# Performance work log

Measured on AMD Instinct MI355X. Metric: run time of the kernel, lower is better.

Reference implementation:

```python
import jax, jax.numpy as jnp
import numpy as np

N_NODES = 800_000
N_FRAGS = 100_000
N_ROOTS = 2_000
NODE_FEATS = 86
HIDDEN = 128
MAX_BROKEN = 6
OUT_DIM = MAX_BROKEN * 2 + 1  # 13
MLP_IN = HIDDEN * 3 + OUT_DIM  # 397


def _lin_init(key, fan_in, fan_out):
    k1, k2 = jax.random.split(key)
    bound = 1.0 / np.sqrt(fan_in)
    W = jax.random.uniform(k1, (fan_in, fan_out), jnp.float32, -bound, bound)
    b = jax.random.uniform(k2, (fan_out,), jnp.float32, -bound, bound)
    return W, b


def setup_inputs() -> dict:
    key = jax.random.key(0)
    ks = jax.random.split(key, 16)
    node_h = jax.random.normal(ks[0], (N_NODES, NODE_FEATS), jnp.float32)
    segment_ids = jnp.sort(jax.random.randint(ks[1], (N_NODES,), 0, N_FRAGS))
    root_repr = jax.random.normal(ks[2], (N_ROOTS, NODE_FEATS), jnp.float32)
    ind_maps = jax.random.randint(ks[3], (N_FRAGS,), 0, N_ROOTS)
    broken = jax.random.randint(ks[4], (N_FRAGS,), 0, OUT_DIM)
    W_root, b_root = _lin_init(ks[5], NODE_FEATS, HIDDEN)
    W_in, b_in = _lin_init(ks[6], NODE_FEATS, HIDDEN)
    W_g1, b_g1 = _lin_init(ks[7], HIDDEN, HIDDEN)
    W_g2, b_g2 = _lin_init(ks[8], HIDDEN, HIDDEN)
    W_m1, b_m1 = _lin_init(ks[9], MLP_IN, HIDDEN)
    W_m2, b_m2 = _lin_init(ks[10], HIDDEN, HIDDEN)
    W_out, b_out = _lin_init(ks[11], HIDDEN, OUT_DIM)
    W_attn, b_attn = _lin_init(ks[12], HIDDEN, OUT_DIM)
    return dict(node_h=node_h, segment_ids=segment_ids, root_repr=root_repr,
                ind_maps=ind_maps, broken=broken,
                W_root=W_root, b_root=b_root, W_in=W_in, b_in=b_in,
                W_g1=W_g1, b_g1=b_g1, W_g2=W_g2, b_g2=b_g2,
                W_m1=W_m1, b_m1=b_m1, W_m2=W_m2, b_m2=b_m2,
                W_out=W_out, b_out=b_out, W_attn=W_attn, b_attn=b_attn)


def _segment_mean(x, seg_ids, num_segments):
    sums = jax.ops.segment_sum(x, seg_ids, num_segments=num_segments)
    counts = jax.ops.segment_sum(jnp.ones((x.shape[0],), x.dtype), seg_ids,
                                 num_segments=num_segments)
    return sums / jnp.maximum(counts, 1.0)[:, None]


def reference(node_h, segment_ids, root_repr, ind_maps, broken,
              W_root, b_root, W_in, b_in, W_g1, b_g1, W_g2, b_g2,
              W_m1, b_m1, W_m2, b_m2, W_out, b_out, W_attn, b_attn):
    # root encoder: Linear + ReLU (dropout=0)
    root_emb = jax.nn.relu(root_repr @ W_root + b_root)        # [R, H]
    ext_root = root_emb[ind_maps]                              # [F, H] gather
    # node input + 2 GNN (nodewise Linear+ReLU fallback) layers
    frag_h = node_h @ W_in + b_in                              # [N, H]
    frag_h = jax.nn.relu(frag_h @ W_g1 + b_g1)
    frag_h = jax.nn.relu(frag_h @ W_g2 + b_g2)
    # ragged mean-pool per fragment graph (dgl.mean_nodes)
    avg_frags = _segment_mean(frag_h, segment_ids, N_FRAGS)    # [F, H]
    # one-hot of clamped broken-bond counts
    broken_oh = jax.nn.one_hot(jnp.clip(broken, 0, MAX_BROKEN * 2), OUT_DIM,
                               dtype=frag_h.dtype)             # [F, 13]
    cat = jnp.concatenate([ext_root, ext_root - avg_frags, avg_frags,
                           broken_oh], axis=-1)                # [F, 397]
    hidden = jax.nn.relu(jax.nn.relu(cat @ W_m1 + b_m1) @ W_m2 + b_m2)
    output = jax.nn.sigmoid(hidden @ W_out + b_out)            # [F, 13]
    attn_weights = hidden @ W_attn + b_attn                    # [F, 13]
    return output, attn_weights
```

## Files before the change

### kernel.cpp

```cpp
#include <hip/hip_runtime.h>
#include <math.h>

typedef __attribute__((ext_vector_type(8))) short short8;
typedef __attribute__((ext_vector_type(4))) float float4v;

__device__ __forceinline__ unsigned short f2bf(float f) {
    union { float f; unsigned u; } v; v.f = f;
    return (unsigned short)((v.u + 0x7fffu + ((v.u >> 16) & 1u)) >> 16);
}

template<int KP>
__device__ __forceinline__ void mfma_gemm(const unsigned short* acts, int astr,
                                          const unsigned short* __restrict__ WT,
                                          const float* __restrict__ bias,
                                          unsigned short* wbuf, int tid,
                                          float4v acc[8])
{
    const int lane = tid & 63, w = tid >> 6, col0 = lane & 15, q = lane >> 4;
#pragma unroll
    for (int t = 0; t < 8; ++t) {
        float b = bias[t * 16 + col0];
        acc[t] = (float4v){b, b, b, b};
    }
    const unsigned short* arow = acts + (w * 16 + col0) * astr + q * 8;
    for (int kc = 0; kc < KP; kc += 64) {
        const int CS = (KP - kc) < 64 ? (KP - kc) : 64;
        __syncthreads();
        const int tpr = CS >> 3;
        for (int it = tid; it < 128 * tpr; it += 256) {
            int c = it / tpr, kk = (it - c * tpr) << 3;
            *(float4*)(wbuf + c * 72 + kk) =
                *(const float4*)(WT + (size_t)c * KP + kc + kk);
        }
        __syncthreads();
        for (int ks = 0; ks < CS; ks += 32) {
            short8 a = *(const short8*)(arow + kc + ks);
#pragma unroll
            for (int t = 0; t < 8; ++t) {
                short8 b = *(const short8*)(wbuf + (t * 16 + col0) * 72 + ks + q * 8);
                acc[t] = __builtin_amdgcn_mfma_f32_16x16x32_bf16(a, b, acc[t], 0, 0, 0);
            }
        }
    }
}

__device__ __forceinline__ void store_bf16(const float4v acc[8], unsigned short* out,
                                           int ostr, int tid, bool relu)
{
    const int lane = tid & 63, w = tid >> 6, col0 = lane & 15, q = lane >> 4;
#pragma unroll
    for (int t = 0; t < 8; ++t)
#pragma unroll
        for (int r = 0; r < 4; ++r) {
            float v = acc[t][r];
            if (relu) v = fmaxf(v, 0.0f);
            out[(w * 16 + q * 4 + r) * ostr + t * 16 + col0] = f2bf(v);
        }
}

__global__ void prep_kernel(const float* __restrict__ W_in, const float* __restrict__ W_g1,
                            const float* __restrict__ W_g2, const float* __restrict__ W_m1,
                            const float* __restrict__ W_m2, const float* __restrict__ W_out,
                            const float* __restrict__ W_attn, unsigned short* __restrict__ wt)
{
    int i = blockIdx.x * 256 + threadIdx.x;
    unsigned short* WT_in = wt;
    unsigned short* WT_g1 = WT_in + 12288;
    unsigned short* WT_g2 = WT_g1 + 16384;
    unsigned short* WT_m1 = WT_g2 + 16384;
    unsigned short* WT_m2 = WT_m1 + 53248;
    unsigned short* WT_h  = WT_m2 + 16384;
    if (i < 12288) { int n = i / 96, k = i - n * 96;
        WT_in[i] = (k < 86) ? f2bf(W_in[k * 128 + n]) : 0; return; }
    i -= 12288;
    if (i < 16384) { int n = i >> 7, k = i & 127;
        WT_g1[i] = f2bf(W_g1[k * 128 + n]); return; }
    i -= 16384;
    if (i < 16384) { int n = i >> 7, k = i & 127;
        WT_g2[i] = f2bf(W_g2[k * 128 + n]); return; }
    i -= 16384;
    if (i < 53248) { int n = i / 416, k = i - n * 416;
        WT_m1[i] = (k < 397) ? f2bf(W_m1[k * 128 + n]) : 0; return; }
    i -= 53248;
    if (i < 16384) { int n = i >> 7, k = i & 127;
        WT_m2[i] = f2bf(W_m2[k * 128 + n]); return; }
    i -= 16384;
    if (i < 4096) { int n = i >> 7, k = i & 127;
        WT_h[i] = (n < 13) ? f2bf(W_out[k * 13 + n])
                           : (n < 26 ? f2bf(W_attn[k * 13 + (n - 13)]) : 0); }
}

__global__ void root_kernel(const float* __restrict__ root_repr,
                            const float* __restrict__ W_root,
                            const float* __restrict__ b_root,
                            float* __restrict__ root_emb)
{
    __shared__ float x[86];
    const int r = blockIdx.x, tid = threadIdx.x;
    if (tid < 86) x[tid] = root_repr[(size_t)r * 86 + tid];
    __syncthreads();
    float acc = b_root[tid];
    for (int k = 0; k < 86; ++k)
        acc = fmaf(x[k], W_root[k * 128 + tid], acc);
    root_emb[(size_t)r * 128 + tid] = fmaxf(acc, 0.0f);
}

__global__ __launch_bounds__(256, 3)
void node_kernel(const float* __restrict__ node_h, const int* __restrict__ seg_ids,
                 const unsigned short* __restrict__ WT_in, const float* __restrict__ b_in,
                 const unsigned short* __restrict__ WT_g1, const float* __restrict__ b_g1,
                 const unsigned short* __restrict__ WT_g2, const float* __restrict__ b_g2,
                 float* __restrict__ frag_sum, float* __restrict__ frag_cnt)
{
    __shared__ __align__(16) unsigned char smem[53248];
    __shared__ int segs[64];
    unsigned short* wbuf = (unsigned short*)smem;
    unsigned short* P1   = (unsigned short*)(smem + 18432);
    unsigned short* P0   = (unsigned short*)(smem + 35840);
    float* finalF = (float*)smem;

    const int tid = threadIdx.x;
    const long n0 = (long)blockIdx.x * 64;

    if (tid < 64) {
        int s = seg_ids[n0 + tid];
        segs[tid] = s;
        atomicAdd(&frag_cnt[s], 1.0f);
    }
    for (int idx = tid; idx < 64 * 86; idx += 256) {
        int n = idx / 86, k = idx - n * 86;
        P0[n * 104 + k] = f2bf(node_h[(n0 + n) * 86 + k]);
    }
    for (int idx = tid; idx < 64 * 10; idx += 256) {
        int n = idx / 10, k = idx - n * 10;
        P0[n * 104 + 86 + k] = 0;
    }
    float4v acc[8];
    mfma_gemm<96>(P0, 104, WT_in, b_in, wbuf, tid, acc);
    store_bf16(acc, P1, 136, tid, false);
    mfma_gemm<128>(P1, 136, WT_g1, b_g1, wbuf, tid, acc);
    store_bf16(acc, P0, 136, tid, true);
    mfma_gemm<128>(P0, 136, WT_g2, b_g2, wbuf, tid, acc);
    __syncthreads();
    {
        const int lane = tid & 63, w = tid >> 6, col0 = lane & 15, q = lane >> 4;
#pragma unroll
        for (int t = 0; t < 8; ++t)
#pragma unroll
            for (int r = 0; r < 4; ++r)
                finalF[(w * 16 + q * 4 + r) * 129 + t * 16 + col0] = fmaxf(acc[t][r], 0.0f);
    }
    __syncthreads();
    {
        const int c = tid & 127, r0 = (tid >> 7) * 32;
        int cur = segs[r0];
        float run = 0.0f;
        for (int n = r0; n < r0 + 32; ++n) {
            int s = segs[n];
            if (s != cur) {
                atomicAdd(&frag_sum[(size_t)cur * 128 + c], run);
                run = 0.0f; cur = s;
            }
            run += finalF[n * 129 + c];
        }
        atomicAdd(&frag_sum[(size_t)cur * 128 + c], run);
    }
}

__global__ __launch_bounds__(256, 3)
void frag_kernel(const float* __restrict__ root_emb, const float* __restrict__ frag_sum,
                 const float* __restrict__ frag_cnt, const int* __restrict__ ind_maps,
                 const int* __restrict__ broken,
                 const unsigned short* __restrict__ WT_m1, const float* __restrict__ b_m1,
                 const unsigned short* __restrict__ WT_m2, const float* __restrict__ b_m2,
                 const unsigned short* __restrict__ WT_h,
                 const float* __restrict__ b_out, const float* __restrict__ b_attn,
                 float* __restrict__ out0, float* __restrict__ out1)
{
    __shared__ __align__(16) unsigned char smem[53248];
    unsigned short* wbuf = (unsigned short*)smem;
    unsigned short* h1 = (unsigned short*)(smem + 18432);
    unsigned short* h2 = (unsigned short*)(smem + 35840);
    const int tid = threadIdx.x;
    const int lane = tid & 63, w = tid >> 6, col0 = lane & 15, q = lane >> 4;
    const long f0 = (long)blockIdx.x * 64;
    const int m = w * 16 + col0;
    int fc = (int)(f0 + m); if (fc > 99999) fc = 99999;
    const int rid = ind_maps[fc];
    const float inv = 1.0f / fmaxf(frag_cnt[fc], 1.0f);
    int bi = broken[fc]; bi = bi < 0 ? 0 : (bi > 12 ? 12 : bi);

    float4v acc[8];
#pragma unroll
    for (int t = 0; t < 8; ++t) {
        float b = b_m1[t * 16 + col0];
        acc[t] = (float4v){b, b, b, b};
    }
    for (int kc = 0; kc < 416; kc += 64) {
        const int CS = (416 - kc) < 64 ? (416 - kc) : 64;
        __syncthreads();
        const int tpr = CS >> 3;
        for (int it = tid; it < 128 * tpr; it += 256) {
            int c = it / tpr, kk = (it - c * tpr) << 3;
            *(float4*)(wbuf + c * 72 + kk) =
                *(const float4*)(WT_m1 + (size_t)c * 416 + kc + kk);
        }
        __syncthreads();
        for (int ks = 0; ks < CS; ks += 32) {
            const int k0 = kc + ks + q * 8;
            float av[8];
            if (k0 >= 384) {
#pragma unroll
                for (int i = 0; i < 8; ++i) {
                    int k = k0 + i;
                    av[i] = (k < 397 && (k - 384) == bi) ? 1.0f : 0.0f;
                }
            } else if (k0 < 128) {
                const float4* e = (const float4*)(root_emb + (size_t)rid * 128 + k0);
                float4 e0 = e[0], e1 = e[1];
                av[0] = e0.x; av[1] = e0.y; av[2] = e0.z; av[3] = e0.w;
                av[4] = e1.x; av[5] = e1.y; av[6] = e1.z; av[7] = e1.w;
            } else if (k0 < 256) {
                int kk = k0 - 128;
                const float4* e = (const float4*)(root_emb + (size_t)rid * 128 + kk);
                const float4* s = (const float4*)(frag_sum + (size_t)fc * 128 + kk);
                float4 e0 = e[0], e1 = e[1], s0 = s[0], s1 = s[1];
                av[0] = e0.x - s0.x * inv; av[1] = e0.y - s0.y * inv;
                av[2] = e0.z - s0.z * inv; av[3] = e0.w - s0.w * inv;
                av[4] = e1.x - s1.x * inv; av[5] = e1.y - s1.y * inv;
                av[6] = e1.z - s1.z * inv; av[7] = e1.w - s1.w * inv;
            } else {
                int kk = k0 - 256;
                const float4* s = (const float4*)(frag_sum + (size_t)fc * 128 + kk);
                float4 s0 = s[0], s1 = s[1];
                av[0] = s0.x * inv; av[1] = s0.y * inv; av[2] = s0.z * inv; av[3] = s0.w * inv;
                av[4] = s1.x * inv; av[5] = s1.y * inv; av[6] = s1.z * inv; av[7] = s1.w * inv;
            }
            short8 a;
#pragma unroll
            for (int i = 0; i < 8; ++i) a[i] = (short)f2bf(av[i]);
#pragma unroll
            for (int t = 0; t < 8; ++t) {
                short8 b = *(const short8*)(wbuf + (t * 16 + col0) * 72 + ks + q * 8);
                acc[t] = __builtin_amdgcn_mfma_f32_16x16x32_bf16(a, b, acc[t], 0, 0, 0);
            }
        }
    }
    store_bf16(acc, h1, 136, tid, true);
    mfma_gemm<128>(h1, 136, WT_m2, b_m2, wbuf, tid, acc);
    store_bf16(acc, h2, 136, tid, true);
    __syncthreads();
    float4v hacc[2];
#pragma unroll
    for (int t = 0; t < 2; ++t) {
        int cc = t * 16 + col0;
        float b = cc < 13 ? b_out[cc] : (cc < 26 ? b_attn[cc - 13] : 0.0f);
        hacc[t] = (float4v){b, b, b, b};
    }
#pragma unroll
    for (int ks = 0; ks < 128; ks += 32) {
        short8 a = *(const short8*)(h2 + m * 136 + ks + q * 8);
#pragma unroll
        for (int t = 0; t < 2; ++t) {
            short8 b = *(const short8*)(WT_h + (t * 16 + col0) * 128 + ks + q * 8);
            hacc[t] = __builtin_amdgcn_mfma_f32_16x16x32_bf16(a, b, hacc[t], 0, 0, 0);
        }
    }
#pragma unroll
    for (int t = 0; t < 2; ++t)
#pragma unroll
        for (int r = 0; r < 4; ++r) {
            long ff = f0 + w * 16 + q * 4 + r;
            if (ff < 100000) {
                int cc = t * 16 + col0;
                float v = hacc[t][r];
                if (cc < 13)      out0[ff * 13 + cc] = 1.0f / (1.0f + expf(-v));
                else if (cc < 26) out1[ff * 13 + cc - 13] = v;
            }
        }
}

extern "C" void kernel_launch(void* const* d_in, const int* in_sizes, int n_in,
                              void* d_out, int out_size, void* d_ws, size_t ws_size,
                              hipStream_t stream)
{
    const float* node_h    = (const float*)d_in[0];
    const int*   seg_ids   = (const int*)d_in[1];
    const float* root_repr = (const float*)d_in[2];
    const int*   ind_maps  = (const int*)d_in[3];
    const int*   broken    = (const int*)d_in[4];
    const float* W_root = (const float*)d_in[5];  const float* b_root = (const float*)d_in[6];
    const float* W_in   = (const float*)d_in[7];  const float* b_in   = (const float*)d_in[8];
    const float* W_g1   = (const float*)d_in[9];  const float* b_g1   = (const float*)d_in[10];
    const float* W_g2   = (const float*)d_in[11]; const float* b_g2   = (const float*)d_in[12];
    const float* W_m1   = (const float*)d_in[13]; const float* b_m1   = (const float*)d_in[14];
    const float* W_m2   = (const float*)d_in[15]; const float* b_m2   = (const float*)d_in[16];
    const float* W_out  = (const float*)d_in[17]; const float* b_out  = (const float*)d_in[18];
    const float* W_attn = (const float*)d_in[19]; const float* b_attn = (const float*)d_in[20];

    char* ws = (char*)d_ws;
    float* root_emb = (float*)ws;
    float* frag_sum = (float*)(ws + 1024000);
    float* frag_cnt = (float*)(ws + 52224000);
    unsigned short* wt = (unsigned short*)(ws + 52624000);
    const unsigned short* WT_in = wt;
    const unsigned short* WT_g1 = wt + 12288;
    const unsigned short* WT_g2 = WT_g1 + 16384;
    const unsigned short* WT_m1 = WT_g2 + 16384;
    const unsigned short* WT_m2 = WT_m1 + 53248;
    const unsigned short* WT_h  = WT_m2 + 16384;

    hipMemsetAsync(frag_sum, 0, 51600000, stream);

    float* out0 = (float*)d_out;
    float* out1 = out0 + (size_t)100000 * 13;

    prep_kernel<<<464, 256, 0, stream>>>(W_in, W_g1, W_g2, W_m1, W_m2, W_out, W_attn, wt);
    root_kernel<<<2000, 128, 0, stream>>>(root_repr, W_root, b_root, root_emb);
    node_kernel<<<12500, 256, 0, stream>>>(node_h, seg_ids, WT_in, b_in,
                                           WT_g1, b_g1, WT_g2, b_g2, frag_sum, frag_cnt);
    frag_kernel<<<1563, 256, 0, stream>>>(root_emb, frag_sum, frag_cnt, ind_maps, broken,
                                          WT_m1, b_m1, WT_m2, b_m2, WT_h, b_out, b_attn,
                                          out0, out1);
}
```

Measured before the change: 729.4 us.

## Give each wavefront a full 64-row strip, stream weights from global, drop block syncs

```diff
diff --git a/kernel.cpp b/kernel.cpp
--- a/kernel.cpp
+++ b/kernel.cpp
@@ -3,59 +3,60 @@
 
 typedef __attribute__((ext_vector_type(8))) short short8;
 typedef __attribute__((ext_vector_type(4))) float float4v;
+
+#define AST 136
 
 __device__ __forceinline__ unsigned short f2bf(float f) {
     union { float f; unsigned u; } v; v.f = f;
     return (unsigned short)((v.u + 0x7fffu + ((v.u >> 16) & 1u)) >> 16);
 }
+__device__ __forceinline__ float bf2f(unsigned v) {
+    union { unsigned u; float f; } x; x.u = v << 16; return x.f;
+}
 
 template<int KP>
-__device__ __forceinline__ void mfma_gemm(const unsigned short* acts, int astr,
-                                          const unsigned short* __restrict__ WT,
-                                          const float* __restrict__ bias,
-                                          unsigned short* wbuf, int tid,
-                                          float4v acc[8])
-{
-    const int lane = tid & 63, w = tid >> 6, col0 = lane & 15, q = lane >> 4;
+__device__ __forceinline__ void layerN(const unsigned short* X,
+                                       const unsigned short* __restrict__ WT,
+                                       const float* __restrict__ bias,
+                                       int lane, float4v acc[4][8])
+{
+    const int col0 = lane & 15, q = lane >> 4;
 #pragma unroll
     for (int t = 0; t < 8; ++t) {
         float b = bias[t * 16 + col0];
-        acc[t] = (float4v){b, b, b, b};
-    }
-    const unsigned short* arow = acts + (w * 16 + col0) * astr + q * 8;
-    for (int kc = 0; kc < KP; kc += 64) {
-        const int CS = (KP - kc) < 64 ? (KP - kc) : 64;
-        __syncthreads();
-        const int tpr = CS >> 3;
-        for (int it = tid; it < 128 * tpr; it += 256) {
-            int c = it / tpr, kk = (it - c * tpr) << 3;
-            *(float4*)(wbuf + c * 72 + kk) =
-                *(const float4*)(WT + (size_t)c * KP + kc + kk);
-        }
-        __syncthreads();
-        for (int ks = 0; ks < CS; ks += 32) {
-            short8 a = *(const short8*)(arow + kc + ks);
-#pragma unroll
-            for (int t = 0; t < 8; ++t) {
-                short8 b = *(const short8*)(wbuf + (t * 16 + col0) * 72 + ks + q * 8);
-                acc[t] = __builtin_amdgcn_mfma_f32_16x16x32_bf16(a, b, acc[t], 0, 0, 0);
+#pragma unroll
+        for (int mt = 0; mt < 4; ++mt) acc[mt][t] = (float4v){b, b, b, b};
+    }
+    for (int ks = 0; ks < KP; ks += 32) {
+        const int k0 = ks + q * 8;
+        short8 B[8];
+#pragma unroll
+        for (int t = 0; t < 8; ++t)
+            B[t] = *(const short8*)(WT + (size_t)(t * 16 + col0) * KP + k0);
+#pragma unroll
+        for (int mt = 0; mt < 4; ++mt) {
+            short8 A = *(const short8*)(X + (mt * 16 + col0) * AST + k0);
+#pragma unroll
+            for (int t = 0; t < 8; ++t)
+                acc[mt][t] = __builtin_amdgcn_mfma_f32_16x16x32_bf16(A, B[t], acc[mt][t], 0, 0, 0);
+        }
+    }
+}
+
+__device__ __forceinline__ void storeh(float4v acc[4][8], unsigned short* X,
+                                       int lane, bool relu)
+{
+    const int col0 = lane & 15, q = lane >> 4;
+#pragma unroll
+    for (int mt = 0; mt < 4; ++mt)
+#pragma unroll
+        for (int t = 0; t < 8; ++t)
+#pragma unroll
+            for (int r = 0; r < 4; ++r) {
+                float v = acc[mt][t][r];
+                if (relu) v = fmaxf(v, 0.0f);
+                X[(mt * 16 + q * 4 + r) * AST + t * 16 + col0] = f2bf(v);
             }
-        }
-    }
-}
-
-__device__ __forceinline__ void store_bf16(const float4v acc[8], unsigned short* out,
-                                           int ostr, int tid, bool relu)
-{
-    const int lane = tid & 63, w = tid >> 6, col0 = lane & 15, q = lane >> 4;
-#pragma unroll
-    for (int t = 0; t < 8; ++t)
-#pragma unroll
-        for (int r = 0; r < 4; ++r) {
-            float v = acc[t][r];
-            if (relu) v = fmaxf(v, 0.0f);
-            out[(w * 16 + q * 4 + r) * ostr + t * 16 + col0] = f2bf(v);
-        }
 }
 
 __global__ void prep_kernel(const float* __restrict__ W_in, const float* __restrict__ W_g1,
@@ -105,69 +106,74 @@
     root_emb[(size_t)r * 128 + tid] = fmaxf(acc, 0.0f);
 }
 
-__global__ __launch_bounds__(256, 3)
+__global__ __launch_bounds__(512, 2)
 void node_kernel(const float* __restrict__ node_h, const int* __restrict__ seg_ids,
                  const unsigned short* __restrict__ WT_in, const float* __restrict__ b_in,
                  const unsigned short* __restrict__ WT_g1, const float* __restrict__ b_g1,
                  const unsigned short* __restrict__ WT_g2, const float* __restrict__ b_g2,
                  float* __restrict__ frag_sum, float* __restrict__ frag_cnt)
 {
-    __shared__ __align__(16) unsigned char smem[53248];
-    __shared__ int segs[64];
-    unsigned short* wbuf = (unsigned short*)smem;
-    unsigned short* P1   = (unsigned short*)(smem + 18432);
-    unsigned short* P0   = (unsigned short*)(smem + 35840);
-    float* finalF = (float*)smem;
-
-    const int tid = threadIdx.x;
-    const long n0 = (long)blockIdx.x * 64;
-
-    if (tid < 64) {
-        int s = seg_ids[n0 + tid];
-        segs[tid] = s;
-        atomicAdd(&frag_cnt[s], 1.0f);
-    }
-    for (int idx = tid; idx < 64 * 86; idx += 256) {
-        int n = idx / 86, k = idx - n * 86;
-        P0[n * 104 + k] = f2bf(node_h[(n0 + n) * 86 + k]);
-    }
-    for (int idx = tid; idx < 64 * 10; idx += 256) {
-        int n = idx / 10, k = idx - n * 10;
-        P0[n * 104 + 86 + k] = 0;
-    }
-    float4v acc[8];
-    mfma_gemm<96>(P0, 104, WT_in, b_in, wbuf, tid, acc);
-    store_bf16(acc, P1, 136, tid, false);
-    mfma_gemm<128>(P1, 136, WT_g1, b_g1, wbuf, tid, acc);
-    store_bf16(acc, P0, 136, tid, true);
-    mfma_gemm<128>(P0, 136, WT_g2, b_g2, wbuf, tid, acc);
-    __syncthreads();
+    __shared__ unsigned short abuf[8 * 64 * AST];
+    __shared__ int segs[8 * 64];
+    const int tid = threadIdx.x, wv = tid >> 6, lane = tid & 63;
+    const int strip = blockIdx.x * 8 + wv;
+    if (strip >= 12500) return;
+    const long n0 = (long)strip * 64;
+    unsigned short* X = abuf + wv * (64 * AST);
+    int* sg = segs + wv * 64;
+
+    sg[lane] = seg_ids[n0 + lane];
+
     {
-        const int lane = tid & 63, w = tid >> 6, col0 = lane & 15, q = lane >> 4;
-#pragma unroll
-        for (int t = 0; t < 8; ++t)
-#pragma unroll
-            for (int r = 0; r < 4; ++r)
-                finalF[(w * 16 + q * 4 + r) * 129 + t * 16 + col0] = fmaxf(acc[t][r], 0.0f);
-    }
-    __syncthreads();
-    {
-        const int c = tid & 127, r0 = (tid >> 7) * 32;
-        int cur = segs[r0];
-        float run = 0.0f;
-        for (int n = r0; n < r0 + 32; ++n) {
-            int s = segs[n];
-            if (s != cur) {
-                atomicAdd(&frag_sum[(size_t)cur * 128 + c], run);
-                run = 0.0f; cur = s;
+        const float4* src = (const float4*)(node_h + n0 * 86);
+#pragma unroll
+        for (int j = 0; j < 22; ++j) {
+            int i4 = j * 64 + lane;
+            if (i4 < 1376) {
+                float4 v = src[i4];
+                int e = i4 << 2;
+                int n = e / 86, k = e - n * 86;
+                X[n * AST + k] = f2bf(v.x);
+                int e1 = e + 1; n = e1 / 86; k = e1 - n * 86; X[n * AST + k] = f2bf(v.y);
+                int e2 = e + 2; n = e2 / 86; k = e2 - n * 86; X[n * AST + k] = f2bf(v.z);
+                int e3 = e + 3; n = e3 / 86; k = e3 - n * 86; X[n * AST + k] = f2bf(v.w);
             }
-            run += finalF[n * 129 + c];
-        }
-        atomicAdd(&frag_sum[(size_t)cur * 128 + c], run);
-    }
-}
-
-__global__ __launch_bounds__(256, 3)
+        }
+#pragma unroll
+        for (int j = 0; j < 10; ++j)
+            X[lane * AST + 86 + j] = 0;
+    }
+
+    float4v acc[4][8];
+    layerN<96>(X, WT_in, b_in, lane, acc);
+    storeh(acc, X, lane, false);
+    layerN<128>(X, WT_g1, b_g1, lane, acc);
+    storeh(acc, X, lane, true);
+    layerN<128>(X, WT_g2, b_g2, lane, acc);
+    storeh(acc, X, lane, true);
+
+    const int c0 = lane << 1;
+    float s0 = 0.f, s1 = 0.f, cnt = 0.f;
+    int cur = sg[0];
+    for (int n = 0; n < 64; ++n) {
+        int s = sg[n];
+        if (s != cur) {
+            atomicAdd(&frag_sum[(size_t)cur * 128 + c0], s0);
+            atomicAdd(&frag_sum[(size_t)cur * 128 + c0 + 1], s1);
+            if (lane == 0) atomicAdd(&frag_cnt[cur], cnt);
+            s0 = s1 = cnt = 0.f; cur = s;
+        }
+        unsigned v = *(const unsigned*)(X + n * AST + c0);
+        s0 += bf2f(v & 0xffffu);
+        s1 += bf2f(v >> 16);
+        cnt += 1.f;
+    }
+    atomicAdd(&frag_sum[(size_t)cur * 128 + c0], s0);
+    atomicAdd(&frag_sum[(size_t)cur * 128 + c0 + 1], s1);
+    if (lane == 0) atomicAdd(&frag_cnt[cur], cnt);
+}
+
+__global__ __launch_bounds__(256, 2)
 void frag_kernel(const float* __restrict__ root_emb, const float* __restrict__ frag_sum,
                  const float* __restrict__ frag_cnt, const int* __restrict__ ind_maps,
                  const int* __restrict__ broken,
@@ -177,107 +183,118 @@
                  const float* __restrict__ b_out, const float* __restrict__ b_attn,
                  float* __restrict__ out0, float* __restrict__ out1)
 {
-    __shared__ __align__(16) unsigned char smem[53248];
-    unsigned short* wbuf = (unsigned short*)smem;
-    unsigned short* h1 = (unsigned short*)(smem + 18432);
-    unsigned short* h2 = (unsigned short*)(smem + 35840);
-    const int tid = threadIdx.x;
-    const int lane = tid & 63, w = tid >> 6, col0 = lane & 15, q = lane >> 4;
-    const long f0 = (long)blockIdx.x * 64;
-    const int m = w * 16 + col0;
-    int fc = (int)(f0 + m); if (fc > 99999) fc = 99999;
-    const int rid = ind_maps[fc];
-    const float inv = 1.0f / fmaxf(frag_cnt[fc], 1.0f);
-    int bi = broken[fc]; bi = bi < 0 ? 0 : (bi > 12 ? 12 : bi);
-
-    float4v acc[8];
+    __shared__ unsigned short abuf[4 * 64 * AST];
+    const int tid = threadIdx.x, wv = tid >> 6, lane = tid & 63;
+    const int strip = blockIdx.x * 4 + wv;
+    const long f0 = (long)strip * 64;
+    if (f0 >= 100000) return;
+    unsigned short* X = abuf + wv * (64 * AST);
+    const int col0 = lane & 15, q = lane >> 4;
+
+    int rid[4]; float inv[4]; int bi[4];
+#pragma unroll
+    for (int mt = 0; mt < 4; ++mt) {
+        int fc = (int)f0 + mt * 16 + col0; if (fc > 99999) fc = 99999;
+        rid[mt] = ind_maps[fc];
+        inv[mt] = 1.0f / fmaxf(frag_cnt[fc], 1.0f);
+        int b = broken[fc]; bi[mt] = b < 0 ? 0 : (b > 12 ? 12 : b);
+    }
+
+    float4v acc[4][8];
 #pragma unroll
     for (int t = 0; t < 8; ++t) {
         float b = b_m1[t * 16 + col0];
-        acc[t] = (float4v){b, b, b, b};
-    }
-    for (int kc = 0; kc < 416; kc += 64) {
-        const int CS = (416 - kc) < 64 ? (416 - kc) : 64;
-        __syncthreads();
-        const int tpr = CS >> 3;
-        for (int it = tid; it < 128 * tpr; it += 256) {
-            int c = it / tpr, kk = (it - c * tpr) << 3;
-            *(float4*)(wbuf + c * 72 + kk) =
-                *(const float4*)(WT_m1 + (size_t)c * 416 + kc + kk);
-        }
-        __syncthreads();
-        for (int ks = 0; ks < CS; ks += 32) {
-            const int k0 = kc + ks + q * 8;
+#pragma unroll
+        for (int mt = 0; mt < 4; ++mt) acc[mt][t] = (float4v){b, b, b, b};
+    }
+    for (int ks = 0; ks < 416; ks += 32) {
+        const int k0 = ks + q * 8;
+        short8 B[8];
+#pragma unroll
+        for (int t = 0; t < 8; ++t)
+            B[t] = *(const short8*)(WT_m1 + (size_t)(t * 16 + col0) * 416 + k0);
+#pragma unroll
+        for (int mt = 0; mt < 4; ++mt) {
+            int fc = (int)f0 + mt * 16 + col0; if (fc > 99999) fc = 99999;
             float av[8];
             if (k0 >= 384) {
 #pragma unroll
                 for (int i = 0; i < 8; ++i) {
                     int k = k0 + i;
-                    av[i] = (k < 397 && (k - 384) == bi) ? 1.0f : 0.0f;
+                    av[i] = (k < 397 && (k - 384) == bi[mt]) ? 1.0f : 0.0f;
                 }
             } else if (k0 < 128) {
-                const float4* e = (const float4*)(root_emb + (size_t)rid * 128 + k0);
+                const float4* e = (const float4*)(root_emb + (size_t)rid[mt] * 128 + k0);
                 float4 e0 = e[0], e1 = e[1];
                 av[0] = e0.x; av[1] = e0.y; av[2] = e0.z; av[3] = e0.w;
                 av[4] = e1.x; av[5] = e1.y; av[6] = e1.z; av[7] = e1.w;
             } else if (k0 < 256) {
                 int kk = k0 - 128;
-                const float4* e = (const float4*)(root_emb + (size_t)rid * 128 + kk);
+                const float4* e = (const float4*)(root_emb + (size_t)rid[mt] * 128 + kk);
                 const float4* s = (const float4*)(frag_sum + (size_t)fc * 128 + kk);
                 float4 e0 = e[0], e1 = e[1], s0 = s[0], s1 = s[1];
-                av[0] = e0.x - s0.x * inv; av[1] = e0.y - s0.y * inv;
-                av[2] = e0.z - s0.z * inv; av[3] = e0.w - s0.w * inv;
-                av[4] = e1.x - s1.x * inv; av[5] = e1.y - s1.y * inv;
-                av[6] = e1.z - s1.z * inv; av[7] = e1.w - s1.w * inv;
+                float iv = inv[mt];
+                av[0] = e0.x - s0.x * iv; av[1] = e0.y - s0.y * iv;
+                av[2] = e0.z - s0.z * iv; av[3] = e0.w - s0.w * iv;
+                av[4] = e1.x - s1.x * iv; av[5] = e1.y - s1.y * iv;
+                av[6] = e1.z - s1.z * iv; av[7] = e1.w - s1.w * iv;
             } else {
                 int kk = k0 - 256;
                 const float4* s = (const float4*)(frag_sum + (size_t)fc * 128 + kk);
                 float4 s0 = s[0], s1 = s[1];
-                av[0] = s0.x * inv; av[1] = s0.y * inv; av[2] = s0.z * inv; av[3] = s0.w * inv;
-                av[4] = s1.x * inv; av[5] = s1.y * inv; av[6] = s1.z * inv; av[7] = s1.w * inv;
+                float iv = inv[mt];
+                av[0] = s0.x * iv; av[1] = s0.y * iv; av[2] = s0.z * iv; av[3] = s0.w * iv;
+                av[4] = s1.x * iv; av[5] = s1.y * iv; av[6] = s1.z * iv; av[7] = s1.w * iv;
             }
-            short8 a;
-#pragma unroll
-            for (int i = 0; i < 8; ++i) a[i] = (short)f2bf(av[i]);
-#pragma unroll
-            for (int t = 0; t < 8; ++t) {
-                short8 b = *(const short8*)(wbuf + (t * 16 + col0) * 72 + ks + q * 8);
-                acc[t] = __builtin_amdgcn_mfma_f32_16x16x32_bf16(a, b, acc[t], 0, 0, 0);
-            }
-        }
-    }
-    store_bf16(acc, h1, 136, tid, true);
-    mfma_gemm<128>(h1, 136, WT_m2, b_m2, wbuf, tid, acc);
-    store_bf16(acc, h2, 136, tid, true);
-    __syncthreads();
-    float4v hacc[2];
+            short8 A;
+#pragma unroll
+            for (int i = 0; i < 8; ++i) A[i] = (short)f2bf(av[i]);
+#pragma unroll
+            for (int t = 0; t < 8; ++t)
+                acc[mt][t] = __builtin_amdgcn_mfma_f32_16x16x32_bf16(A, B[t], acc[mt][t], 0, 0, 0);
+        }
+    }
+    storeh(acc, X, lane, true);
+    layerN<128>(X, WT_m2, b_m2, lane, acc);
+    storeh(acc, X, lane, true);
+
+    float4v hacc[4][2];
 #pragma unroll
     for (int t = 0; t < 2; ++t) {
         int cc = t * 16 + col0;
         float b = cc < 13 ? b_out[cc] : (cc < 26 ? b_attn[cc - 13] : 0.0f);
-        hacc[t] = (float4v){b, b, b, b};
+#pragma unroll
+        for (int mt = 0; mt < 4; ++mt) hacc[mt][t] = (float4v){b, b, b, b};
     }
 #pragma unroll
     for (int ks = 0; ks < 128; ks += 32) {
-        short8 a = *(const short8*)(h2 + m * 136 + ks + q * 8);
-#pragma unroll
-        for (int t = 0; t < 2; ++t) {
-            short8 b = *(const short8*)(WT_h + (t * 16 + col0) * 128 + ks + q * 8);
-            hacc[t] = __builtin_amdgcn_mfma_f32_16x16x32_bf16(a, b, hacc[t], 0, 0, 0);
-        }
-    }
-#pragma unroll
-    for (int t = 0; t < 2; ++t)
-#pragma unroll
-        for (int r = 0; r < 4; ++r) {
-            long ff = f0 + w * 16 + q * 4 + r;
-            if (ff < 100000) {
+        const int k0 = ks + q * 8;
+        short8 B2[2];
+#pragma unroll
+        for (int t = 0; t < 2; ++t)
+            B2[t] = *(const short8*)(WT_h + (t * 16 + col0) * 128 + k0);
+#pragma unroll
+        for (int mt = 0; mt < 4; ++mt) {
+            short8 A = *(const short8*)(X + (mt * 16 + col0) * AST + k0);
+#pragma unroll
+            for (int t = 0; t < 2; ++t)
+                hacc[mt][t] = __builtin_amdgcn_mfma_f32_16x16x32_bf16(A, B2[t], hacc[mt][t], 0, 0, 0);
+        }
+    }
+#pragma unroll
+    for (int mt = 0; mt < 4; ++mt)
+#pragma unroll
+        for (int t = 0; t < 2; ++t)
+#pragma unroll
+            for (int r = 0; r < 4; ++r) {
+                long ff = f0 + mt * 16 + q * 4 + r;
                 int cc = t * 16 + col0;
-                float v = hacc[t][r];
-                if (cc < 13)      out0[ff * 13 + cc] = 1.0f / (1.0f + expf(-v));
-                else if (cc < 26) out1[ff * 13 + cc - 13] = v;
+                if (ff < 100000) {
+                    float v = hacc[mt][t][r];
+                    if (cc < 13)      out0[ff * 13 + cc] = 1.0f / (1.0f + expf(-v));
+                    else if (cc < 26) out1[ff * 13 + cc - 13] = v;
+                }
             }
-        }
 }
 
 extern "C" void kernel_launch(void* const* d_in, const int* in_sizes, int n_in,
@@ -317,9 +334,9 @@
 
     prep_kernel<<<464, 256, 0, stream>>>(W_in, W_g1, W_g2, W_m1, W_m2, W_out, W_attn, wt);
     root_kernel<<<2000, 128, 0, stream>>>(root_repr, W_root, b_root, root_emb);
-    node_kernel<<<12500, 256, 0, stream>>>(node_h, seg_ids, WT_in, b_in,
-                                           WT_g1, b_g1, WT_g2, b_g2, frag_sum, frag_cnt);
-    frag_kernel<<<1563, 256, 0, stream>>>(root_emb, frag_sum, frag_cnt, ind_maps, broken,
-                                          WT_m1, b_m1, WT_m2, b_m2, WT_h, b_out, b_attn,
-                                          out0, out1);
-}
+    node_kernel<<<1563, 512, 0, stream>>>(node_h, seg_ids, WT_in, b_in,
+                                          WT_g1, b_g1, WT_g2, b_g2, frag_sum, frag_cnt);
+    frag_kernel<<<391, 256, 0, stream>>>(root_emb, frag_sum, frag_cnt, ind_maps, broken,
+                                         WT_m1, b_m1, WT_m2, b_m2, WT_h, b_out, b_attn,
+                                         out0, out1);
+}
```

After: 693.6 us. -4.9%, faster.

## Retile MFMA layers per wave and cut atomics in segment pooling

Applied to the files above, without the earlier changes.

```diff
diff --git a/kernel.cpp b/kernel.cpp
--- a/kernel.cpp
+++ b/kernel.cpp
@@ -3,59 +3,62 @@
 
 typedef __attribute__((ext_vector_type(8))) short short8;
 typedef __attribute__((ext_vector_type(4))) float float4v;
+
+#define AST 136
+#define CST 424
 
 __device__ __forceinline__ unsigned short f2bf(float f) {
     union { float f; unsigned u; } v; v.f = f;
     return (unsigned short)((v.u + 0x7fffu + ((v.u >> 16) & 1u)) >> 16);
 }
+__device__ __forceinline__ float bf2f(unsigned v) {
+    union { unsigned u; float f; } x; x.u = v << 16; return x.f;
+}
 
 template<int KP>
-__device__ __forceinline__ void mfma_gemm(const unsigned short* acts, int astr,
-                                          const unsigned short* __restrict__ WT,
-                                          const float* __restrict__ bias,
-                                          unsigned short* wbuf, int tid,
-                                          float4v acc[8])
-{
-    const int lane = tid & 63, w = tid >> 6, col0 = lane & 15, q = lane >> 4;
-#pragma unroll
-    for (int t = 0; t < 8; ++t) {
-        float b = bias[t * 16 + col0];
-        acc[t] = (float4v){b, b, b, b};
-    }
-    const unsigned short* arow = acts + (w * 16 + col0) * astr + q * 8;
-    for (int kc = 0; kc < KP; kc += 64) {
-        const int CS = (KP - kc) < 64 ? (KP - kc) : 64;
-        __syncthreads();
-        const int tpr = CS >> 3;
-        for (int it = tid; it < 128 * tpr; it += 256) {
-            int c = it / tpr, kk = (it - c * tpr) << 3;
-            *(float4*)(wbuf + c * 72 + kk) =
-                *(const float4*)(WT + (size_t)c * KP + kc + kk);
-        }
-        __syncthreads();
-        for (int ks = 0; ks < CS; ks += 32) {
-            short8 a = *(const short8*)(arow + kc + ks);
-#pragma unroll
-            for (int t = 0; t < 8; ++t) {
-                short8 b = *(const short8*)(wbuf + (t * 16 + col0) * 72 + ks + q * 8);
-                acc[t] = __builtin_amdgcn_mfma_f32_16x16x32_bf16(a, b, acc[t], 0, 0, 0);
+__device__ __forceinline__ void layer2t(const unsigned short* X, int astr,
+                                        const unsigned short* __restrict__ WT,
+                                        const float* __restrict__ bias,
+                                        int lane, int tb, float4v acc[4][2])
+{
+    const int col0 = lane & 15, q = lane >> 4;
+#pragma unroll
+    for (int t = 0; t < 2; ++t) {
+        float b = bias[(tb + t) * 16 + col0];
+#pragma unroll
+        for (int mt = 0; mt < 4; ++mt) acc[mt][t] = (float4v){b, b, b, b};
+    }
+#pragma unroll
+    for (int ks = 0; ks < KP; ks += 32) {
+        const int k0 = ks + q * 8;
+        short8 B[2];
+#pragma unroll
+        for (int t = 0; t < 2; ++t)
+            B[t] = *(const short8*)(WT + (size_t)((tb + t) * 16 + col0) * KP + k0);
+#pragma unroll
+        for (int mt = 0; mt < 4; ++mt) {
+            short8 A = *(const short8*)(X + (mt * 16 + col0) * astr + k0);
+#pragma unroll
+            for (int t = 0; t < 2; ++t)
+                acc[mt][t] = __builtin_amdgcn_mfma_f32_16x16x32_bf16(A, B[t], acc[mt][t], 0, 0, 0);
+        }
+    }
+}
+
+__device__ __forceinline__ void store2t(float4v acc[4][2], unsigned short* Y,
+                                        int lane, int tb, bool relu)
+{
+    const int col0 = lane & 15, q = lane >> 4;
+#pragma unroll
+    for (int mt = 0; mt < 4; ++mt)
+#pragma unroll
+        for (int t = 0; t < 2; ++t)
+#pragma unroll
+            for (int r = 0; r < 4; ++r) {
+                float v = acc[mt][t][r];
+                if (relu) v = fmaxf(v, 0.0f);
+                Y[(mt * 16 + q * 4 + r) * AST + (tb + t) * 16 + col0] = f2bf(v);
             }
-        }
-    }
-}
-
-__device__ __forceinline__ void store_bf16(const float4v acc[8], unsigned short* out,
-                                           int ostr, int tid, bool relu)
-{
-    const int lane = tid & 63, w = tid >> 6, col0 = lane & 15, q = lane >> 4;
-#pragma unroll
-    for (int t = 0; t < 8; ++t)
-#pragma unroll
-        for (int r = 0; r < 4; ++r) {
-            float v = acc[t][r];
-            if (relu) v = fmaxf(v, 0.0f);
-            out[(w * 16 + q * 4 + r) * ostr + t * 16 + col0] = f2bf(v);
-        }
 }
 
 __global__ void prep_kernel(const float* __restrict__ W_in, const float* __restrict__ W_g1,
@@ -105,69 +108,86 @@
     root_emb[(size_t)r * 128 + tid] = fmaxf(acc, 0.0f);
 }
 
-__global__ __launch_bounds__(256, 3)
+__global__ __launch_bounds__(256, 4)
 void node_kernel(const float* __restrict__ node_h, const int* __restrict__ seg_ids,
                  const unsigned short* __restrict__ WT_in, const float* __restrict__ b_in,
                  const unsigned short* __restrict__ WT_g1, const float* __restrict__ b_g1,
                  const unsigned short* __restrict__ WT_g2, const float* __restrict__ b_g2,
                  float* __restrict__ frag_sum, float* __restrict__ frag_cnt)
 {
-    __shared__ __align__(16) unsigned char smem[53248];
+    __shared__ __align__(16) unsigned short X[64 * AST];
+    __shared__ __align__(16) unsigned short Y[64 * AST];
     __shared__ int segs[64];
-    unsigned short* wbuf = (unsigned short*)smem;
-    unsigned short* P1   = (unsigned short*)(smem + 18432);
-    unsigned short* P0   = (unsigned short*)(smem + 35840);
-    float* finalF = (float*)smem;
-
-    const int tid = threadIdx.x;
+    const int tid = threadIdx.x, wv = tid >> 6, lane = tid & 63, tb = wv * 2;
     const long n0 = (long)blockIdx.x * 64;
 
-    if (tid < 64) {
-        int s = seg_ids[n0 + tid];
-        segs[tid] = s;
-        atomicAdd(&frag_cnt[s], 1.0f);
-    }
-    for (int idx = tid; idx < 64 * 86; idx += 256) {
-        int n = idx / 86, k = idx - n * 86;
-        P0[n * 104 + k] = f2bf(node_h[(n0 + n) * 86 + k]);
-    }
-    for (int idx = tid; idx < 64 * 10; idx += 256) {
-        int n = idx / 10, k = idx - n * 10;
-        P0[n * 104 + 86 + k] = 0;
-    }
-    float4v acc[8];
-    mfma_gemm<96>(P0, 104, WT_in, b_in, wbuf, tid, acc);
-    store_bf16(acc, P1, 136, tid, false);
-    mfma_gemm<128>(P1, 136, WT_g1, b_g1, wbuf, tid, acc);
-    store_bf16(acc, P0, 136, tid, true);
-    mfma_gemm<128>(P0, 136, WT_g2, b_g2, wbuf, tid, acc);
-    __syncthreads();
+    if (tid < 64) segs[tid] = seg_ids[n0 + tid];
     {
-        const int lane = tid & 63, w = tid >> 6, col0 = lane & 15, q = lane >> 4;
-#pragma unroll
-        for (int t = 0; t < 8; ++t)
-#pragma unroll
-            for (int r = 0; r < 4; ++r)
-                finalF[(w * 16 + q * 4 + r) * 129 + t * 16 + col0] = fmaxf(acc[t][r], 0.0f);
-    }
-    __syncthreads();
+        const float4* src = (const float4*)(node_h + n0 * 86);
+#pragma unroll
+        for (int j = 0; j < 6; ++j) {
+            int i4 = j * 256 + tid;
+            if (i4 < 1376) {
+                float4 v = src[i4];
+                int e = i4 << 2;
+                int n = e / 86, k = e - n * 86;
+                X[n * AST + k] = f2bf(v.x);
+                int e1 = e + 1; n = e1 / 86; k = e1 - n * 86; X[n * AST + k] = f2bf(v.y);
+                int e2 = e + 2; n = e2 / 86; k = e2 - n * 86; X[n * AST + k] = f2bf(v.z);
+                int e3 = e + 3; n = e3 / 86; k = e3 - n * 86; X[n * AST + k] = f2bf(v.w);
+            }
+        }
+        for (int idx = tid; idx < 640; idx += 256) {
+            int n = idx / 10, k = idx - n * 10;
+            X[n * AST + 86 + k] = 0;
+        }
+    }
+    __syncthreads();
+
+    float4v acc[4][2];
+    layer2t<96>(X, AST, WT_in, b_in, lane, tb, acc);
+    store2t(acc, Y, lane, tb, false);
+    __syncthreads();
+    layer2t<128>(Y, AST, WT_g1, b_g1, lane, tb, acc);
+    store2t(acc, X, lane, tb, true);
+    __syncthreads();
+    layer2t<128>(X, AST, WT_g2, b_g2, lane, tb, acc);
+    store2t(acc, Y, lane, tb, true);
+    __syncthreads();
+
     {
-        const int c = tid & 127, r0 = (tid >> 7) * 32;
-        int cur = segs[r0];
-        float run = 0.0f;
+        const int col = tid & 127, half = tid >> 7, r0 = half << 5;
+        const int prevSeg = (half == 1) ? segs[31] : -1;
+        const int nextSeg = (half == 0) ? segs[32] : -1;
+        int cur = segs[r0], runStart = r0;
+        float sum = 0.f, cnt = 0.f;
         for (int n = r0; n < r0 + 32; ++n) {
             int s = segs[n];
             if (s != cur) {
-                atomicAdd(&frag_sum[(size_t)cur * 128 + c], run);
-                run = 0.0f; cur = s;
+                bool bnd = (runStart == r0) && (half == 0 || prevSeg == cur);
+                if (bnd) atomicAdd(&frag_sum[(size_t)cur * 128 + col], sum);
+                else     frag_sum[(size_t)cur * 128 + col] = sum;
+                if (col == 0) {
+                    if (bnd) atomicAdd(&frag_cnt[cur], cnt);
+                    else     frag_cnt[cur] = cnt;
+                }
+                sum = 0.f; cnt = 0.f; cur = s; runStart = n;
             }
-            run += finalF[n * 129 + c];
-        }
-        atomicAdd(&frag_sum[(size_t)cur * 128 + c], run);
-    }
-}
-
-__global__ __launch_bounds__(256, 3)
+            sum += bf2f((unsigned)Y[n * AST + col]);
+            cnt += 1.f;
+        }
+        bool bnd = ((runStart == r0) && (half == 0 || prevSeg == cur))
+                   || (half == 1) || (nextSeg == cur);
+        if (bnd) atomicAdd(&frag_sum[(size_t)cur * 128 + col], sum);
+        else     frag_sum[(size_t)cur * 128 + col] = sum;
+        if (col == 0) {
+            if (bnd) atomicAdd(&frag_cnt[cur], cnt);
+            else     frag_cnt[cur] = cnt;
+        }
+    }
+}
+
+__global__ __launch_bounds__(256, 2)
 void frag_kernel(const float* __restrict__ root_emb, const float* __restrict__ frag_sum,
                  const float* __restrict__ frag_cnt, const int* __restrict__ ind_maps,
                  const int* __restrict__ broken,
@@ -177,79 +197,48 @@
                  const float* __restrict__ b_out, const float* __restrict__ b_attn,
                  float* __restrict__ out0, float* __restrict__ out1)
 {
-    __shared__ __align__(16) unsigned char smem[53248];
-    unsigned short* wbuf = (unsigned short*)smem;
-    unsigned short* h1 = (unsigned short*)(smem + 18432);
-    unsigned short* h2 = (unsigned short*)(smem + 35840);
-    const int tid = threadIdx.x;
-    const int lane = tid & 63, w = tid >> 6, col0 = lane & 15, q = lane >> 4;
+    __shared__ __align__(16) unsigned short cat[64 * CST];
+    __shared__ __align__(16) unsigned short Y[64 * AST];
+    unsigned short* X2 = cat;
+    const int tid = threadIdx.x, wv = tid >> 6, lane = tid & 63, tb = wv * 2;
+    const int col0 = lane & 15, q = lane >> 4;
     const long f0 = (long)blockIdx.x * 64;
-    const int m = w * 16 + col0;
-    int fc = (int)(f0 + m); if (fc > 99999) fc = 99999;
-    const int rid = ind_maps[fc];
-    const float inv = 1.0f / fmaxf(frag_cnt[fc], 1.0f);
-    int bi = broken[fc]; bi = bi < 0 ? 0 : (bi > 12 ? 12 : bi);
-
-    float4v acc[8];
-#pragma unroll
-    for (int t = 0; t < 8; ++t) {
-        float b = b_m1[t * 16 + col0];
-        acc[t] = (float4v){b, b, b, b};
-    }
-    for (int kc = 0; kc < 416; kc += 64) {
-        const int CS = (416 - kc) < 64 ? (416 - kc) : 64;
-        __syncthreads();
-        const int tpr = CS >> 3;
-        for (int it = tid; it < 128 * tpr; it += 256) {
-            int c = it / tpr, kk = (it - c * tpr) << 3;
-            *(float4*)(wbuf + c * 72 + kk) =
-                *(const float4*)(WT_m1 + (size_t)c * 416 + kc + kk);
-        }
-        __syncthreads();
-        for (int ks = 0; ks < CS; ks += 32) {
-            const int k0 = kc + ks + q * 8;
-            float av[8];
-            if (k0 >= 384) {
-#pragma unroll
-                for (int i = 0; i < 8; ++i) {
-                    int k = k0 + i;
-                    av[i] = (k < 397 && (k - 384) == bi) ? 1.0f : 0.0f;
-                }
-            } else if (k0 < 128) {
-                const float4* e = (const float4*)(root_emb + (size_t)rid * 128 + k0);
-                float4 e0 = e[0], e1 = e[1];
-                av[0] = e0.x; av[1] = e0.y; av[2] = e0.z; av[3] = e0.w;
-                av[4] = e1.x; av[5] = e1.y; av[6] = e1.z; av[7] = e1.w;
-            } else if (k0 < 256) {
-                int kk = k0 - 128;
-                const float4* e = (const float4*)(root_emb + (size_t)rid * 128 + kk);
-                const float4* s = (const float4*)(frag_sum + (size_t)fc * 128 + kk);
-                float4 e0 = e[0], e1 = e[1], s0 = s[0], s1 = s[1];
-                av[0] = e0.x - s0.x * inv; av[1] = e0.y - s0.y * inv;
-                av[2] = e0.z - s0.z * inv; av[3] = e0.w - s0.w * inv;
-                av[4] = e1.x - s1.x * inv; av[5] = e1.y - s1.y * inv;
-                av[6] = e1.z - s1.z * inv; av[7] = e1.w - s1.w * inv;
-            } else {
-                int kk = k0 - 256;
-                const float4* s = (const float4*)(frag_sum + (size_t)fc * 128 + kk);
-                float4 s0 = s[0], s1 = s[1];
-                av[0] = s0.x * inv; av[1] = s0.y * inv; av[2] = s0.z * inv; av[3] = s0.w * inv;
-                av[4] = s1.x * inv; av[5] = s1.y * inv; av[6] = s1.z * inv; av[7] = s1.w * inv;
-            }
-            short8 a;
-#pragma unroll
-            for (int i = 0; i < 8; ++i) a[i] = (short)f2bf(av[i]);
-#pragma unroll
-            for (int t = 0; t < 8; ++t) {
-                short8 b = *(const short8*)(wbuf + (t * 16 + col0) * 72 + ks + q * 8);
-                acc[t] = __builtin_amdgcn_mfma_f32_16x16x32_bf16(a, b, acc[t], 0, 0, 0);
-            }
-        }
-    }
-    store_bf16(acc, h1, 136, tid, true);
-    mfma_gemm<128>(h1, 136, WT_m2, b_m2, wbuf, tid, acc);
-    store_bf16(acc, h2, 136, tid, true);
-    __syncthreads();
+
+    {
+        const int m = tid >> 2, j = tid & 3;
+        int fc = (int)f0 + m; if (fc > 99999) fc = 99999;
+        const int rid = ind_maps[fc];
+        const float inv = 1.0f / fmaxf(frag_cnt[fc], 1.0f);
+        unsigned short* row = cat + m * CST;
+#pragma unroll
+        for (int jj = 0; jj < 8; ++jj) {
+            int k = j * 32 + jj * 4;
+            float4 e = *(const float4*)(root_emb + (size_t)rid * 128 + k);
+            float4 s = *(const float4*)(frag_sum + (size_t)fc * 128 + k);
+            float sx = s.x * inv, sy = s.y * inv, sz = s.z * inv, sw = s.w * inv;
+            row[k]     = f2bf(e.x); row[k + 1] = f2bf(e.y);
+            row[k + 2] = f2bf(e.z); row[k + 3] = f2bf(e.w);
+            row[128 + k]     = f2bf(e.x - sx); row[128 + k + 1] = f2bf(e.y - sy);
+            row[128 + k + 2] = f2bf(e.z - sz); row[128 + k + 3] = f2bf(e.w - sw);
+            row[256 + k]     = f2bf(sx); row[256 + k + 1] = f2bf(sy);
+            row[256 + k + 2] = f2bf(sz); row[256 + k + 3] = f2bf(sw);
+        }
+        if (j == 3) {
+            int b = broken[fc]; b = b < 0 ? 0 : (b > 12 ? 12 : b);
+            for (int kk = 0; kk < 32; ++kk)
+                row[384 + kk] = (kk == b) ? 0x3f80 : 0;
+        }
+    }
+    __syncthreads();
+
+    float4v acc[4][2];
+    layer2t<416>(cat, CST, WT_m1, b_m1, lane, tb, acc);
+    store2t(acc, Y, lane, tb, true);
+    __syncthreads();
+    layer2t<128>(Y, AST, WT_m2, b_m2, lane, tb, acc);
+    store2t(acc, X2, lane, tb, true);
+    __syncthreads();
+
     float4v hacc[2];
 #pragma unroll
     for (int t = 0; t < 2; ++t) {
@@ -259,20 +248,21 @@
     }
 #pragma unroll
     for (int ks = 0; ks < 128; ks += 32) {
-        short8 a = *(const short8*)(h2 + m * 136 + ks + q * 8);
+        const int k0 = ks + q * 8;
+        short8 A = *(const short8*)(X2 + (wv * 16 + col0) * AST + k0);
 #pragma unroll
         for (int t = 0; t < 2; ++t) {
-            short8 b = *(const short8*)(WT_h + (t * 16 + col0) * 128 + ks + q * 8);
-            hacc[t] = __builtin_amdgcn_mfma_f32_16x16x32_bf16(a, b, hacc[t], 0, 0, 0);
+            short8 B = *(const short8*)(WT_h + (t * 16 + col0) * 128 + k0);
+            hacc[t] = __builtin_amdgcn_mfma_f32_16x16x32_bf16(A, B, hacc[t], 0, 0, 0);
         }
     }
 #pragma unroll
     for (int t = 0; t < 2; ++t)
 #pragma unroll
         for (int r = 0; r < 4; ++r) {
-            long ff = f0 + w * 16 + q * 4 + r;
+            long ff = f0 + wv * 16 + q * 4 + r;
+            int cc = t * 16 + col0;
             if (ff < 100000) {
-                int cc = t * 16 + col0;
                 float v = hacc[t][r];
                 if (cc < 13)      out0[ff * 13 + cc] = 1.0f / (1.0f + expf(-v));
                 else if (cc < 26) out1[ff * 13 + cc - 13] = v;
```

New measurement: 585.1 us. -19.8%, faster.
